# Kernel optimization log

Hardware: AMD Instinct MI355X
Metric: run time of the kernel (lower is better)

## Reference

```python
import jax, jax.numpy as jnp
import numpy as np

DIM = 512
NUM_HEADS = 8
NUM_BLOCKS = 16
# NOTE: original code computes head_dim from FULL dim (before the reduce layer),
# so scale = (dim // num_heads) ** -0.5 = 64 ** -0.5, even though the actual
# per-head dim after reduce is 32. We preserve this quirk faithfully.
SCALE = (DIM // NUM_HEADS) ** -0.5


def setup_inputs() -> dict:
    key = jax.random.key(0)
    ks = jax.random.split(key, 5)
    B, N = 4, 4096
    C = DIM // 2
    x = jax.random.normal(ks[0], (B, N, DIM), dtype=jnp.float32)
    reduce_w = jax.random.normal(ks[1], (DIM, C), dtype=jnp.float32) * (DIM ** -0.5)
    qkv_w = jax.random.normal(ks[2], (C, 3 * C), dtype=jnp.float32) * (C ** -0.5)
    proj_w = jax.random.normal(ks[3], (C, DIM), dtype=jnp.float32) * (C ** -0.5)
    proj_b = jnp.zeros((DIM,), dtype=jnp.float32)
    return {"x": x, "reduce_w": reduce_w, "qkv_w": qkv_w,
            "proj_w": proj_w, "proj_b": proj_b}


def reference(x, reduce_w, qkv_w, proj_w, proj_b):
    B, N, _ = x.shape
    xr = x @ reduce_w                      # [B, N, C]  (C = dim/2)
    C = xr.shape[-1]
    H = NUM_HEADS
    d = C // H
    qkv = (xr @ qkv_w).reshape(B, N, 3, H, d).transpose(2, 0, 3, 1, 4)  # [3,B,H,N,d]
    q, k, v = qkv[0], qkv[1], qkv[2]
    bs = N // NUM_BLOCKS                   # block (chunk) size
    # block-diagonal local attention: reshape seq into independent blocks
    qb = q.reshape(B, H, NUM_BLOCKS, bs, d)
    kb = k.reshape(B, H, NUM_BLOCKS, bs, d)
    vb = v.reshape(B, H, NUM_BLOCKS, bs, d)
    attn = jnp.einsum('bhnqd,bhnkd->bhnqk', qb, kb) * SCALE
    attn = jax.nn.softmax(attn, axis=-1)
    ob = jnp.einsum('bhnqk,bhnkd->bhnqd', attn, vb)   # [B,H,Nb,bs,d]
    # torch: per-block transpose(1,2) then cat on dim=1 -> [B, N, H, d]
    o = ob.transpose(0, 2, 3, 1, 4).reshape(B, N, C)
    return o @ proj_w + proj_b
```

## Files before the change

kernel.cpp:

```cpp
#include <hip/hip_runtime.h>
#include <hip/hip_fp16.h>

typedef _Float16 half_t;
typedef _Float16 f16x8 __attribute__((ext_vector_type(8)));
typedef __fp16 fp16x2 __attribute__((ext_vector_type(2)));
typedef float f32x4 __attribute__((ext_vector_type(4)));

#define MFMA_F16(a, b, c) __builtin_amdgcn_mfma_f32_16x16x32_f16((a), (b), (c), 0, 0, 0)

static __device__ inline unsigned pkrtz(float a, float b) {
    union { fp16x2 h; unsigned u; } c;
    c.h = __builtin_amdgcn_cvt_pkrtz(a, b);
    return c.u;
}

__device__ __forceinline__ void gload16(const half_t* g, half_t* l) {
    __builtin_amdgcn_global_load_lds(
        (const __attribute__((address_space(1))) void*)g,
        (__attribute__((address_space(3))) void*)l, 16, 0, 0);
}

__global__ void prep(const float* __restrict__ x, const float* __restrict__ rw,
                     const float* __restrict__ qw, const float* __restrict__ pw,
                     half_t* __restrict__ x_h, half_t* __restrict__ rw_h,
                     half_t* __restrict__ qw_t, half_t* __restrict__ pw_t) {
    int bid = blockIdx.x;
    if (bid < 4096) {
        int i8 = (bid * 256 + threadIdx.x) * 8;
        float4 a = *(const float4*)(x + i8);
        float4 b = *(const float4*)(x + i8 + 4);
        f16x8 v;
        v[0] = (half_t)a.x; v[1] = (half_t)a.y; v[2] = (half_t)a.z; v[3] = (half_t)a.w;
        v[4] = (half_t)b.x; v[5] = (half_t)b.y; v[6] = (half_t)b.z; v[7] = (half_t)b.w;
        *(f16x8*)(x_h + i8) = v;
        return;
    }
    int idx = (bid - 4096) * 256 + threadIdx.x;
    if (idx < 131072) {
        rw_h[idx] = (half_t)rw[idx];
    } else if (idx < 327680) {
        int j = idx - 131072;
        int r = j / 768, c = j - r * 768;
        float v = qw[j];
        if (c < 256) v *= 0.125f;
        qw_t[c * 256 + r] = (half_t)v;
    } else if (idx < 458752) {
        int j = idx - 327680;
        int r = j >> 9, c = j & 511;
        pw_t[c * 256 + r] = (half_t)pw[j];
    }
}

template <int EPI, int K>
__global__ __launch_bounds__(256) void gemm_f16(
    const half_t* __restrict__ A, const half_t* __restrict__ Bt,
    void* __restrict__ Dst, const float* __restrict__ bias) {
    constexpr int nkt = K >> 6;
    __shared__ __align__(16) char smem[2 * 24576];

    const int tid = threadIdx.x;
    const int lane = tid & 63, w = tid >> 6;
    const int l15 = lane & 15, l4 = lane >> 4;
    const int wrow = (w >> 1) * 32, wcol = (w & 1) * 64;
    const int bm0 = blockIdx.x * 64;
    const int bn0 = blockIdx.y * 128;

    const half_t* srcA[2];
#pragma unroll
    for (int i = 0; i < 2; ++i) {
        int J = w * 128 + i * 64 + lane;
        int row = J >> 3, c = (J & 7) ^ (row & 7);
        srcA[i] = A + (size_t)(bm0 + row) * K + c * 8;
    }
    const half_t* srcB[4];
#pragma unroll
    for (int i = 0; i < 4; ++i) {
        int J = w * 256 + i * 64 + lane;
        int row = J >> 3, c = (J & 7) ^ (row & 7);
        srcB[i] = Bt + (size_t)(bn0 + row) * K + c * 8;
    }

    auto STAGE = [&](int kt, int b) {
        char* As = smem + b * 24576;
        char* Bs = As + 8192;
#pragma unroll
        for (int i = 0; i < 2; ++i)
            gload16(srcA[i] + kt * 64, (half_t*)(As + (w * 2 + i) * 1024));
#pragma unroll
        for (int i = 0; i < 4; ++i)
            gload16(srcB[i] + kt * 64, (half_t*)(Bs + (w * 4 + i) * 1024));
    };

    f32x4 acc[2][4];
#pragma unroll
    for (int i = 0; i < 2; ++i)
#pragma unroll
        for (int j = 0; j < 4; ++j) acc[i][j] = (f32x4){0.f, 0.f, 0.f, 0.f};

    const int pa = (l15 & 7) << 4;

    STAGE(0, 0);
    for (int kt = 0; kt < nkt; ++kt) {
        if (kt + 1 < nkt) {
            STAGE(kt + 1, (kt + 1) & 1);
            asm volatile("s_waitcnt vmcnt(6)" ::: "memory");
        } else {
            asm volatile("s_waitcnt vmcnt(0)" ::: "memory");
        }
        __builtin_amdgcn_s_barrier();
        __builtin_amdgcn_sched_barrier(0);

        const char* As = smem + (kt & 1) * 24576;
        const char* Bs = As + 8192;
#pragma unroll
        for (int ki = 0; ki < 2; ++ki) {
            f16x8 af[2], bf[4];
#pragma unroll
            for (int mi = 0; mi < 2; ++mi) {
                int row = wrow + mi * 16 + l15;
                af[mi] = *(const f16x8*)(As + row * 128 + (((ki * 4 + l4) << 4) ^ pa));
            }
#pragma unroll
            for (int nj = 0; nj < 4; ++nj) {
                int row = wcol + nj * 16 + l15;
                bf[nj] = *(const f16x8*)(Bs + row * 128 + (((ki * 4 + l4) << 4) ^ pa));
            }
#pragma unroll
            for (int mi = 0; mi < 2; ++mi)
#pragma unroll
                for (int nj = 0; nj < 4; ++nj)
                    acc[mi][nj] = MFMA_F16(af[mi], bf[nj], acc[mi][nj]);
        }
        __builtin_amdgcn_sched_barrier(0);
        __builtin_amdgcn_s_barrier();
    }

#pragma unroll
    for (int mi = 0; mi < 2; ++mi) {
#pragma unroll
        for (int nj = 0; nj < 4; ++nj) {
#pragma unroll
            for (int reg = 0; reg < 4; ++reg) {
                int grow = bm0 + wrow + mi * 16 + l4 * 4 + reg;
                int gcol = bn0 + wcol + nj * 16 + l15;
                float val = acc[mi][nj][reg];
                if (EPI == 1) {
                    int t = gcol >> 8, h = (gcol >> 5) & 7, dd = gcol & 31;
                    int b = grow >> 12, n = grow & 4095;
                    int blk = n >> 8, r = n & 255;
                    size_t base = (size_t)t * 4194304 +
                                  (size_t)((((b << 3) + h) << 4) + blk) * 8192;
                    size_t idx = (t == 2) ? base + (size_t)dd * 256 + r
                                          : base + (size_t)r * 32 + dd;
                    ((half_t*)Dst)[idx] = (half_t)val;
                } else if (EPI == 2) {
                    ((float*)Dst)[(size_t)grow * 512 + gcol] = val + bias[gcol];
                } else {
                    ((half_t*)Dst)[(size_t)grow * 512 + gcol] = (half_t)val;
                }
            }
        }
    }
}

__global__ __launch_bounds__(256, 4) void attn_f16(const half_t* __restrict__ qkv_ws,
                                                   half_t* __restrict__ o_ws) {
    const int bid = blockIdx.x;
    const int blkid = ((bid >> 4) << 3) | (bid & 7);
    const int hh = (bid >> 3) & 1;
    const int b = blkid >> 7, h = (blkid >> 4) & 7, blk = blkid & 15;
    const half_t* Q  = qkv_ws + (size_t)blkid * 8192;
    const half_t* Kp = qkv_ws + 4194304 + (size_t)blkid * 8192;
    const half_t* VT = qkv_ws + 8388608 + (size_t)blkid * 8192;

    const int tid = threadIdx.x, lane = tid & 63, w = tid >> 6;
    const int l15 = lane & 15, l4 = lane >> 4;
    const int qb = hh * 128 + w * 32;

    f16x8 aq[2];
    aq[0] = *(const f16x8*)(Q + (qb + l15) * 32 + l4 * 8);
    aq[1] = *(const f16x8*)(Q + (qb + 16 + l15) * 32 + l4 * 8);

    float m_run[2] = {-1e30f, -1e30f}, s_run[2] = {0.f, 0.f};
    f32x4 acc_o[2][2];
#pragma unroll
    for (int qg = 0; qg < 2; ++qg)
#pragma unroll
        for (int fo = 0; fo < 2; ++fo) acc_o[qg][fo] = (f32x4){0.f, 0.f, 0.f, 0.f};
    const f32x4 zero4 = (f32x4){0.f, 0.f, 0.f, 0.f};

    for (int kt = 0; kt < 4; ++kt) {
        f16x8 ka[4];
#pragma unroll
        for (int t = 0; t < 4; ++t)
            ka[t] = *(const f16x8*)(Kp + (kt * 64 + t * 16 + l15) * 32 + l4 * 8);
        f16x8 bv[2][2];
#pragma unroll
        for (int c = 0; c < 2; ++c)
#pragma unroll
            for (int fo = 0; fo < 2; ++fo)
                bv[c][fo] = *(const f16x8*)(VT + (fo * 16 + l15) * 256 + kt * 64 + c * 32 + l4 * 8);

#pragma unroll
        for (int qg = 0; qg < 2; ++qg) {
            f32x4 st[4];
#pragma unroll
            for (int t = 0; t < 4; ++t) st[t] = MFMA_F16(ka[t], aq[qg], zero4);

            float mt = -1e30f;
#pragma unroll
            for (int t = 0; t < 4; ++t)
#pragma unroll
                for (int r = 0; r < 4; ++r) mt = fmaxf(mt, st[t][r]);
            mt = fmaxf(mt, __shfl_xor(mt, 16));
            mt = fmaxf(mt, __shfl_xor(mt, 32));

            float mn = fmaxf(m_run[qg], mt);
            float corr = __expf(m_run[qg] - mn);
            m_run[qg] = mn;

            float p[4][4];
            float ps = 0.f;
#pragma unroll
            for (int t = 0; t < 4; ++t)
#pragma unroll
                for (int r = 0; r < 4; ++r) {
                    float e = __expf(st[t][r] - mn);
                    p[t][r] = e;
                    ps += e;
                }
            ps += __shfl_xor(ps, 16);
            ps += __shfl_xor(ps, 32);
            s_run[qg] = s_run[qg] * corr + ps;

            float corrs[4];
#pragma unroll
            for (int r = 0; r < 4; ++r) corrs[r] = __shfl(corr, (l4 << 2) | r);
#pragma unroll
            for (int fo = 0; fo < 2; ++fo)
#pragma unroll
                for (int r = 0; r < 4; ++r) acc_o[qg][fo][r] *= corrs[r];

#pragma unroll
            for (int c = 0; c < 2; ++c) {
                unsigned pk0[2], pk1[2];
#pragma unroll
                for (int rp = 0; rp < 2; ++rp) {
                    pk0[rp] = pkrtz(p[2 * c][2 * rp], p[2 * c][2 * rp + 1]);
                    pk1[rp] = pkrtz(p[2 * c + 1][2 * rp], p[2 * c + 1][2 * rp + 1]);
                }
                union { unsigned u[4]; f16x8 v; } au;
#pragma unroll
                for (int j = 0; j < 4; ++j) {
                    int src = l15 + ((((l4 & 1) << 1) + (j >> 1)) << 4);
                    unsigned g0 = (unsigned)__shfl((int)pk0[j & 1], src);
                    unsigned g1 = (unsigned)__shfl((int)pk1[j & 1], src);
                    au.u[j] = (l4 < 2) ? g0 : g1;
                }
#pragma unroll
                for (int fo = 0; fo < 2; ++fo)
                    acc_o[qg][fo] = MFMA_F16(au.v, bv[c][fo], acc_o[qg][fo]);
            }
        }
    }

#pragma unroll
    for (int qg = 0; qg < 2; ++qg) {
        float inv = 1.f / s_run[qg];
        float sinv[4];
#pragma unroll
        for (int r = 0; r < 4; ++r) sinv[r] = __shfl(inv, (l4 << 2) | r);
#pragma unroll
        for (int fo = 0; fo < 2; ++fo)
#pragma unroll
            for (int r = 0; r < 4; ++r) {
                int grow = b * 4096 + blk * 256 + qb + qg * 16 + l4 * 4 + r;
                o_ws[(size_t)grow * 256 + h * 32 + fo * 16 + l15] =
                    (half_t)(acc_o[qg][fo][r] * sinv[r]);
            }
    }
}

extern "C" void kernel_launch(void* const* d_in, const int* in_sizes, int n_in,
                              void* d_out, int out_size, void* d_ws, size_t ws_size,
                              hipStream_t stream) {
    const float* x        = (const float*)d_in[0];
    const float* reduce_w = (const float*)d_in[1];
    const float* qkv_w    = (const float*)d_in[2];
    const float* proj_w   = (const float*)d_in[3];
    const float* proj_b   = (const float*)d_in[4];
    char* ws = (char*)d_ws;

    half_t* qkv_ws = (half_t*)ws;
    half_t* o_buf  = (half_t*)(ws + 25165824);
    half_t* rw_h   = (half_t*)(ws + 33554432);
    half_t* qw_t   = (half_t*)(ws + 33816576);
    half_t* pw_t   = (half_t*)(ws + 34209792);
    half_t* Wt     = (half_t*)(ws + 34471936);
    half_t* x_h    = (half_t*)(ws + 35258368);

    prep<<<5888, 256, 0, stream>>>(x, reduce_w, qkv_w, proj_w, x_h, rw_h, qw_t, pw_t);

    gemm_f16<3, 256><<<dim3(12, 4), 256, 0, stream>>>(qw_t, rw_h, Wt, nullptr);
    gemm_f16<1, 512><<<dim3(256, 6), 256, 0, stream>>>(x_h, Wt, qkv_ws, nullptr);
    attn_f16<<<1024, 256, 0, stream>>>(qkv_ws, o_buf);
    gemm_f16<2, 256><<<dim3(256, 4), 256, 0, stream>>>(o_buf, pw_t, d_out, proj_b);
}
```

Before: 74.68 us.

## Fuse weight-product GEMM into prep kernel and triple-buffer GEMM pipeline

Computes the combined weight product (qkv_w^T times reduce_w^T) inside the prep kernel, converting fp32 to fp16 on the fly. This drops the separate weight GEMM launch and the intermediate fp16 copies of reduce_w and qkv_w. The proj_w transpose now goes through an LDS tile so both reads and writes are coalesced. The main GEMMs switch from double to triple buffering, keeping two stages of loads in flight at the cost of more LDS per block, which may lower occupancy.

```diff
diff --git a/kernel.cpp b/kernel.cpp
--- a/kernel.cpp
+++ b/kernel.cpp
@@ -20,35 +20,117 @@
         (__attribute__((address_space(3))) void*)l, 16, 0, 0);
 }
 
-__global__ void prep(const float* __restrict__ x, const float* __restrict__ rw,
-                     const float* __restrict__ qw, const float* __restrict__ pw,
-                     half_t* __restrict__ x_h, half_t* __restrict__ rw_h,
-                     half_t* __restrict__ qw_t, half_t* __restrict__ pw_t) {
-    int bid = blockIdx.x;
-    if (bid < 4096) {
-        int i8 = (bid * 256 + threadIdx.x) * 8;
-        float4 a = *(const float4*)(x + i8);
-        float4 b = *(const float4*)(x + i8 + 4);
-        f16x8 v;
-        v[0] = (half_t)a.x; v[1] = (half_t)a.y; v[2] = (half_t)a.z; v[3] = (half_t)a.w;
-        v[4] = (half_t)b.x; v[5] = (half_t)b.y; v[6] = (half_t)b.z; v[7] = (half_t)b.w;
-        *(f16x8*)(x_h + i8) = v;
+__global__ __launch_bounds__(256) void prep(
+    const float* __restrict__ x, const float* __restrict__ qw,
+    const float* __restrict__ rw, const float* __restrict__ pw,
+    half_t* __restrict__ x_h, half_t* __restrict__ pw_t, half_t* __restrict__ Wt) {
+    __shared__ __align__(16) char smem[24576];
+    const int bid = blockIdx.x, tid = threadIdx.x;
+
+    if (bid < 48) {
+        char* As = smem;
+        char* Bs = smem + 8192;
+        const int M0 = (bid % 12) * 64, N0 = (bid / 12) * 128;
+        const int lane = tid & 63, w = tid >> 6;
+        const int l15 = lane & 15, l4 = lane >> 4;
+        const int wrow = (w >> 1) * 32, wcol = (w & 1) * 64;
+        const int pa = (l15 & 7) << 4;
+
+        f32x4 acc[2][4];
+#pragma unroll
+        for (int i = 0; i < 2; ++i)
+#pragma unroll
+            for (int j = 0; j < 4; ++j) acc[i][j] = (f32x4){0.f, 0.f, 0.f, 0.f};
+
+        for (int kc = 0; kc < 4; ++kc) {
+            int c0 = kc * 64;
+            __syncthreads();
+#pragma unroll
+            for (int i = 0; i < 2; ++i) {
+                int j = tid + i * 256;
+                int row = j >> 3, e8 = (j & 7) * 8;
+                float s = (M0 + row) < 256 ? 0.125f : 1.f;
+                f16x8 v;
+#pragma unroll
+                for (int e = 0; e < 8; ++e)
+                    v[e] = (half_t)(qw[(size_t)(c0 + e8 + e) * 768 + M0 + row] * s);
+                *(f16x8*)(As + row * 128 + ((e8 * 2) ^ ((row & 7) << 4))) = v;
+            }
+#pragma unroll
+            for (int i = 0; i < 4; ++i) {
+                int j = tid + i * 256;
+                int row = j >> 3, e8 = (j & 7) * 8;
+                const float* p = rw + (size_t)(N0 + row) * 256 + c0 + e8;
+                float4 u0 = *(const float4*)p;
+                float4 u1 = *(const float4*)(p + 4);
+                f16x8 v;
+                v[0] = (half_t)u0.x; v[1] = (half_t)u0.y;
+                v[2] = (half_t)u0.z; v[3] = (half_t)u0.w;
+                v[4] = (half_t)u1.x; v[5] = (half_t)u1.y;
+                v[6] = (half_t)u1.z; v[7] = (half_t)u1.w;
+                *(f16x8*)(Bs + row * 128 + ((e8 * 2) ^ ((row & 7) << 4))) = v;
+            }
+            __syncthreads();
+#pragma unroll
+            for (int ki = 0; ki < 2; ++ki) {
+                f16x8 af[2], bf[4];
+#pragma unroll
+                for (int mi = 0; mi < 2; ++mi) {
+                    int row = wrow + mi * 16 + l15;
+                    af[mi] = *(const f16x8*)(As + row * 128 + (((ki * 4 + l4) << 4) ^ pa));
+                }
+#pragma unroll
+                for (int nj = 0; nj < 4; ++nj) {
+                    int row = wcol + nj * 16 + l15;
+                    bf[nj] = *(const f16x8*)(Bs + row * 128 + (((ki * 4 + l4) << 4) ^ pa));
+                }
+#pragma unroll
+                for (int mi = 0; mi < 2; ++mi)
+#pragma unroll
+                    for (int nj = 0; nj < 4; ++nj)
+                        acc[mi][nj] = MFMA_F16(af[mi], bf[nj], acc[mi][nj]);
+            }
+        }
+#pragma unroll
+        for (int mi = 0; mi < 2; ++mi)
+#pragma unroll
+            for (int nj = 0; nj < 4; ++nj)
+#pragma unroll
+                for (int reg = 0; reg < 4; ++reg) {
+                    int grow = M0 + wrow + mi * 16 + l4 * 4 + reg;
+                    int gcol = N0 + wcol + nj * 16 + l15;
+                    Wt[(size_t)grow * 512 + gcol] = (half_t)acc[mi][nj][reg];
+                }
         return;
     }
-    int idx = (bid - 4096) * 256 + threadIdx.x;
-    if (idx < 131072) {
-        rw_h[idx] = (half_t)rw[idx];
-    } else if (idx < 327680) {
-        int j = idx - 131072;
-        int r = j / 768, c = j - r * 768;
-        float v = qw[j];
-        if (c < 256) v *= 0.125f;
-        qw_t[c * 256 + r] = (half_t)v;
-    } else if (idx < 458752) {
-        int j = idx - 327680;
-        int r = j >> 9, c = j & 511;
-        pw_t[c * 256 + r] = (half_t)pw[j];
-    }
+
+    if (bid < 80) {
+        half_t* tile = (half_t*)smem;
+        int t = bid - 48;
+        int R0 = (t >> 3) * 64, C0 = (t & 7) * 64;
+#pragma unroll
+        for (int e = 0; e < 16; ++e) {
+            int idx = tid + e * 256;
+            int r = idx >> 6, c = idx & 63;
+            tile[r * 72 + c] = (half_t)pw[(size_t)(R0 + r) * 512 + C0 + c];
+        }
+        __syncthreads();
+#pragma unroll
+        for (int e = 0; e < 16; ++e) {
+            int idx = tid + e * 256;
+            int c = idx >> 6, r = idx & 63;
+            pw_t[(size_t)(C0 + c) * 256 + R0 + r] = tile[r * 72 + c];
+        }
+        return;
+    }
+
+    int i8 = ((bid - 80) * 256 + tid) * 8;
+    float4 a = *(const float4*)(x + i8);
+    float4 b = *(const float4*)(x + i8 + 4);
+    f16x8 v;
+    v[0] = (half_t)a.x; v[1] = (half_t)a.y; v[2] = (half_t)a.z; v[3] = (half_t)a.w;
+    v[4] = (half_t)b.x; v[5] = (half_t)b.y; v[6] = (half_t)b.z; v[7] = (half_t)b.w;
+    *(f16x8*)(x_h + i8) = v;
 }
 
 template <int EPI, int K>
@@ -56,7 +138,7 @@
     const half_t* __restrict__ A, const half_t* __restrict__ Bt,
     void* __restrict__ Dst, const float* __restrict__ bias) {
     constexpr int nkt = K >> 6;
-    __shared__ __align__(16) char smem[2 * 24576];
+    __shared__ __align__(16) char smem[3 * 24576];
 
     const int tid = threadIdx.x;
     const int lane = tid & 63, w = tid >> 6;
@@ -80,8 +162,8 @@
         srcB[i] = Bt + (size_t)(bn0 + row) * K + c * 8;
     }
 
-    auto STAGE = [&](int kt, int b) {
-        char* As = smem + b * 24576;
+    auto STAGE = [&](int kt) {
+        char* As = smem + (kt % 3) * 24576;
         char* Bs = As + 8192;
 #pragma unroll
         for (int i = 0; i < 2; ++i)
@@ -99,10 +181,14 @@
 
     const int pa = (l15 & 7) << 4;
 
-    STAGE(0, 0);
+    STAGE(0);
+    STAGE(1);
+#pragma unroll
     for (int kt = 0; kt < nkt; ++kt) {
-        if (kt + 1 < nkt) {
-            STAGE(kt + 1, (kt + 1) & 1);
+        if (kt + 2 < nkt) {
+            STAGE(kt + 2);
+            asm volatile("s_waitcnt vmcnt(12)" ::: "memory");
+        } else if (kt + 1 < nkt) {
             asm volatile("s_waitcnt vmcnt(6)" ::: "memory");
         } else {
             asm volatile("s_waitcnt vmcnt(0)" ::: "memory");
@@ -110,7 +196,7 @@
         __builtin_amdgcn_s_barrier();
         __builtin_amdgcn_sched_barrier(0);
 
-        const char* As = smem + (kt & 1) * 24576;
+        const char* As = smem + (kt % 3) * 24576;
         const char* Bs = As + 8192;
 #pragma unroll
         for (int ki = 0; ki < 2; ++ki) {
@@ -153,10 +239,8 @@
                     size_t idx = (t == 2) ? base + (size_t)dd * 256 + r
                                           : base + (size_t)r * 32 + dd;
                     ((half_t*)Dst)[idx] = (half_t)val;
-                } else if (EPI == 2) {
+                } else {
                     ((float*)Dst)[(size_t)grow * 512 + gcol] = val + bias[gcol];
-                } else {
-                    ((half_t*)Dst)[(size_t)grow * 512 + gcol] = (half_t)val;
                 }
             }
         }
@@ -293,15 +377,11 @@
 
     half_t* qkv_ws = (half_t*)ws;
     half_t* o_buf  = (half_t*)(ws + 25165824);
-    half_t* rw_h   = (half_t*)(ws + 33554432);
-    half_t* qw_t   = (half_t*)(ws + 33816576);
-    half_t* pw_t   = (half_t*)(ws + 34209792);
-    half_t* Wt     = (half_t*)(ws + 34471936);
-    half_t* x_h    = (half_t*)(ws + 35258368);
-
-    prep<<<5888, 256, 0, stream>>>(x, reduce_w, qkv_w, proj_w, x_h, rw_h, qw_t, pw_t);
-
-    gemm_f16<3, 256><<<dim3(12, 4), 256, 0, stream>>>(qw_t, rw_h, Wt, nullptr);
+    half_t* pw_t   = (half_t*)(ws + 33554432);
+    half_t* Wt     = (half_t*)(ws + 33816576);
+    half_t* x_h    = (half_t*)(ws + 34603008);
+
+    prep<<<4176, 256, 0, stream>>>(x, qkv_w, reduce_w, proj_w, x_h, pw_t, Wt);
     gemm_f16<1, 512><<<dim3(256, 6), 256, 0, stream>>>(x_h, Wt, qkv_ws, nullptr);
     attn_f16<<<1024, 256, 0, stream>>>(qkv_ws, o_buf);
     gemm_f16<2, 256><<<dim3(256, 4), 256, 0, stream>>>(o_buf, pw_t, d_out, proj_b);
```

Result: no change. 74.16 us (-0.7%).
